# Kernel tuning notes

Measured on AMD Instinct MI355X. Metric: run time of the kernel, lower is better.

## Reference

```python
import jax, jax.numpy as jnp
import numpy as np

B, T = 16384, 64
VOCAB, D, HD, FF = 10, 3, 4, 2
EPS = 1e-6


def _rms(x, w):
    return x * jax.lax.rsqrt(jnp.mean(x * x, axis=-1, keepdims=True) + EPS) * w


def _rope(x, theta=3.0):
    # x: [..., T, HD]; interleaved rotary, matching the torch RotaryEmbedding
    t = jnp.arange(x.shape[-2], dtype=x.dtype)
    inv_freq = 1.0 / theta ** (jnp.arange(0, HD, 2, dtype=x.dtype) / HD)  # [HD/2]
    freqs = jnp.outer(t, inv_freq)                                        # [T, HD/2]
    cos_f, sin_f = jnp.cos(freqs), jnp.sin(freqs)
    x1, x2 = x[..., ::2], x[..., 1::2]
    rot = jnp.stack([x1 * cos_f - x2 * sin_f, x1 * sin_f + x2 * cos_f], axis=-1)
    return rot.reshape(x.shape)


def setup_inputs() -> dict:
    key = jax.random.key(0)
    ks = jax.random.split(key, 12)
    f32 = jnp.float32
    return {
        "idx": jax.random.randint(ks[0], (B, T), 0, VOCAB, dtype=jnp.int32),
        "arc_A": jnp.asarray(2.5, f32),
        "arc_start": jnp.asarray(-1.2, f32),
        "arc_stride": jnp.asarray(0.29, f32),
        "w_ln1": jnp.ones((D,), f32) + 0.1 * jax.random.normal(ks[1], (D,), f32),
        "w_ln2": jnp.ones((D,), f32) + 0.1 * jax.random.normal(ks[2], (D,), f32),
        "w_lnf": jnp.ones((D,), f32) + 0.1 * jax.random.normal(ks[3], (D,), f32),
        "w_qn": jnp.ones((HD,), f32) + 0.1 * jax.random.normal(ks[4], (HD,), f32),
        "Wq": jax.random.normal(ks[5], (HD, D), f32) * 0.5,
        "Wk": jax.random.normal(ks[6], (HD, D), f32) * 0.5,
        "Wg": jax.random.normal(ks[7], (FF, D), f32) * 0.5,
        "Wu": jax.random.normal(ks[8], (FF, D), f32) * 0.5,
        "Wd": jax.random.normal(ks[9], (D, FF), f32) * 0.5,
    }


def reference(idx, arc_A, arc_start, arc_stride, w_ln1, w_ln2, w_lnf, w_qn,
              Wq, Wk, Wg, Wu, Wd):
    dt = arc_A.dtype
    # circular-arc token embedding table [VOCAB, 2]
    digits = jnp.arange(VOCAB, dtype=dt)
    angles = arc_start + digits * arc_stride
    table = jnp.stack([arc_A * jnp.cos(angles), arc_A * jnp.sin(angles)], axis=1)

    tok = table[idx]                                              # [B,T,2]
    pe = jnp.sin(jnp.arange(T, dtype=dt) * jnp.exp(jnp.asarray(-np.log(10000.0), dt)))
    pos = jnp.broadcast_to(pe[None, :, None], (idx.shape[0], T, 1))
    x = jnp.concatenate([tok, pos], axis=-1)                      # [B,T,3]

    h = _rms(x, w_ln1)
    q = _rms(h @ Wq.T, w_qn)                                      # [B,T,HD]
    k = _rms(h @ Wk.T, w_qn)
    v = h @ Wk.T                                                  # v = k pre-norm? no: v = k.clone() BEFORE q_norm
    q = _rope(q)
    k = _rope(k)

    scale = HD ** (-0.5)
    scores = jnp.einsum("btd,bsd->bts", q, k) * scale             # [B,T,T]
    causal = jnp.triu(jnp.ones((T, T), dtype=bool), k=1)
    scores = jnp.where(causal, -jnp.inf, scores)
    attn = jax.nn.softmax(scores, axis=-1)
    out = jnp.einsum("bts,bsd->btd", attn, v)                     # [B,T,HD]

    x = x + out @ Wq                                              # F.linear(out, Wq.T) == out @ Wq
    h = _rms(x, w_ln2)
    x = x + (jax.nn.silu(h @ Wg.T) * (h @ Wu.T)) @ Wd.T
    x = _rms(x, w_lnf)
    return x[..., :2] @ table.T                                   # [B,T,VOCAB]
```

## Files before the change

kernel.cpp:

```cpp
#include <hip/hip_runtime.h>
#include <math.h>


namespace {
constexpr int kVocab = 10;
constexpr float kEps = 1e-6f;
constexpr int kWaves = 4;

typedef __attribute__((ext_vector_type(8)))  short short8;
typedef __attribute__((ext_vector_type(16))) float float16;

constexpr int kOffQh  = 0;
constexpr int kOffQl  = 512;
constexpr int kOffKh  = 1024;
constexpr int kOffKl  = 1536;
constexpr int kOffVt  = 2048;
constexpr int kOffO   = 3200;
constexpr int kWaveLds = 4736;
constexpr int kVtP = 72;
constexpr int kOP  = 76;

__device__ __forceinline__ unsigned bf16_1(float a) {
    return (__float_as_uint(a) + 0x8000u) >> 16;
}
__device__ __forceinline__ unsigned pk_bf16(float a, float b) {
    const unsigned au = __float_as_uint(a) + 0x8000u;
    const unsigned bu = __float_as_uint(b) + 0x8000u;
    return (au >> 16) | (bu & 0xffff0000u);
}
__device__ __forceinline__ float bf_lo(unsigned u) { return __uint_as_float(u << 16); }
__device__ __forceinline__ float bf_hi(unsigned u) { return __uint_as_float(u & 0xffff0000u); }

__device__ __forceinline__ float16 mfma(short8 a, short8 b, float16 c) {
    return __builtin_amdgcn_mfma_f32_32x32x16_bf16(a, b, c, 0, 0, 0);
}

__device__ __forceinline__ short8 tok_frag(const char* wbase, int off, int tok, bool lo_half) {
    uint2 r = *(const uint2*)(wbase + off + tok * 8);
    uint4 t;
    t.x = lo_half ? r.x : 0u;
    t.y = lo_half ? r.y : 0u;
    t.z = 0u; t.w = 0u;
    return __builtin_bit_cast(short8, t);
}

template<bool MASKED>
__device__ __forceinline__ void exp_pack(const float16& S, unsigned* out, int m) {
#pragma unroll
    for (int i = 0; i < 8; ++i) {
        const int r0 = 2 * i, r1 = 2 * i + 1;
        float sa = S[r0], sb = S[r1];
        if (MASKED) {
            sa = (((r0 & 3) + 8 * (r0 >> 2)) <= m) ? sa : -INFINITY;
            sb = (((r1 & 3) + 8 * (r1 >> 2)) <= m) ? sb : -INFINITY;
        }
        out[i] = pk_bf16(__builtin_amdgcn_exp2f(sa), __builtin_amdgcn_exp2f(sb));
    }
}

__device__ __forceinline__ short8 af(const unsigned* p) {
    uint4 t;
    t.x = p[0]; t.y = p[1]; t.z = p[2]; t.w = p[3];
    return __builtin_bit_cast(short8, t);
}
__device__ __forceinline__ short8 ld8(const void* p) {
    return __builtin_bit_cast(short8, *(const uint4*)p);
}

__global__ __launch_bounds__(256, 4) void adder_model_kernel(
    const int* __restrict__ idx,
    const float* __restrict__ p_arcA,
    const float* __restrict__ p_arcStart,
    const float* __restrict__ p_arcStride,
    const float* __restrict__ w_ln1,
    const float* __restrict__ w_ln2,
    const float* __restrict__ w_lnf,
    const float* __restrict__ w_qn,
    const float* __restrict__ Wq,
    const float* __restrict__ Wk,
    const float* __restrict__ Wg,
    const float* __restrict__ Wu,
    const float* __restrict__ Wd,
    float* __restrict__ out)
{
    __shared__ __align__(16) char smem[kWaves][kWaveLds];
    __shared__ __align__(16) float table_s[kVocab * 2];

    const int lane = threadIdx.x & 63;
    const int wid  = threadIdx.x >> 6;
    char* wbase = &smem[wid][0];

    if (threadIdx.x < kVocab) {
        const float ang = p_arcStart[0] + (float)threadIdx.x * p_arcStride[0];
        const float A = p_arcA[0];
        table_s[2 * threadIdx.x]     = A * __cosf(ang);
        table_s[2 * threadIdx.x + 1] = A * __sinf(ang);
    }
    __syncthreads();

    const float t_f = (float)lane;
    const float pe  = __sinf(t_f * 1e-4f);
    const float c0  = __cosf(t_f);
    const float s0  = __sinf(t_f);
    const float ang1 = t_f * 0.57735026918962576f;
    const float c1  = __cosf(ang1);
    const float s1  = __sinf(ang1);

    const float wl1_0 = w_ln1[0], wl1_1 = w_ln1[1], wl1_2 = w_ln1[2];
    const float wl2_0 = w_ln2[0], wl2_1 = w_ln2[1], wl2_2 = w_ln2[2];
    const float wlf0 = w_lnf[0], wlf1 = w_lnf[1];
    const float wqn0 = w_qn[0], wqn1 = w_qn[1], wqn2 = w_qn[2], wqn3 = w_qn[3];
    const float Wq00 = Wq[0],  Wq01 = Wq[1],  Wq02 = Wq[2];
    const float Wq10 = Wq[3],  Wq11 = Wq[4],  Wq12 = Wq[5];
    const float Wq20 = Wq[6],  Wq21 = Wq[7],  Wq22 = Wq[8];
    const float Wq30 = Wq[9],  Wq31 = Wq[10], Wq32 = Wq[11];
    const float Wk00 = Wk[0],  Wk01 = Wk[1],  Wk02 = Wk[2];
    const float Wk10 = Wk[3],  Wk11 = Wk[4],  Wk12 = Wk[5];
    const float Wk20 = Wk[6],  Wk21 = Wk[7],  Wk22 = Wk[8];
    const float Wk30 = Wk[9],  Wk31 = Wk[10], Wk32 = Wk[11];
    const float Wg00 = Wg[0],  Wg01 = Wg[1],  Wg02 = Wg[2];
    const float Wg10 = Wg[3],  Wg11 = Wg[4],  Wg12 = Wg[5];
    const float Wu00 = Wu[0],  Wu01 = Wu[1],  Wu02 = Wu[2];
    const float Wu10 = Wu[3],  Wu11 = Wu[4],  Wu12 = Wu[5];
    const float Wd00 = Wd[0],  Wd01 = Wd[1];
    const float Wd10 = Wd[2],  Wd11 = Wd[3];
    const float Wd20 = Wd[4],  Wd21 = Wd[5];

    const int row = (int)blockIdx.x * kWaves + wid;

    const int tix = idx[(size_t)row * 64 + lane];
    const float2 emb = *(const float2*)(table_s + 2 * tix);
    const float x0i = emb.x, x1i = emb.y, x2i = pe;

    const float r1 = __builtin_amdgcn_rsqf((x0i*x0i + x1i*x1i + x2i*x2i) * (1.0f/3.0f) + kEps);
    const float h0 = x0i * r1 * wl1_0;
    const float h1 = x1i * r1 * wl1_1;
    const float h2 = x2i * r1 * wl1_2;

    const float qp0 = h0*Wq00 + h1*Wq01 + h2*Wq02;
    const float qp1 = h0*Wq10 + h1*Wq11 + h2*Wq12;
    const float qp2 = h0*Wq20 + h1*Wq21 + h2*Wq22;
    const float qp3 = h0*Wq30 + h1*Wq31 + h2*Wq32;
    const float v0 = h0*Wk00 + h1*Wk01 + h2*Wk02;
    const float v1 = h0*Wk10 + h1*Wk11 + h2*Wk12;
    const float v2 = h0*Wk20 + h1*Wk21 + h2*Wk22;
    const float v3 = h0*Wk30 + h1*Wk31 + h2*Wk32;

    const float rq = __builtin_amdgcn_rsqf((qp0*qp0 + qp1*qp1 + qp2*qp2 + qp3*qp3) * 0.25f + kEps);
    const float rk = __builtin_amdgcn_rsqf((v0*v0 + v1*v1 + v2*v2 + v3*v3) * 0.25f + kEps);
    const float qn0 = qp0*rq*wqn0, qn1 = qp1*rq*wqn1, qn2 = qp2*rq*wqn2, qn3 = qp3*rq*wqn3;
    const float kn0 = v0*rk*wqn0,  kn1 = v1*rk*wqn1,  kn2 = v2*rk*wqn2,  kn3 = v3*rk*wqn3;

    constexpr float kQS = 0.72134752044448170f;
    const float q0 = (qn0*c0 - qn1*s0) * kQS;
    const float q1 = (qn0*s0 + qn1*c0) * kQS;
    const float q2 = (qn2*c1 - qn3*s1) * kQS;
    const float q3 = (qn2*s1 + qn3*c1) * kQS;
    const float k0 = kn0*c0 - kn1*s0;
    const float k1 = kn0*s0 + kn1*c0;
    const float k2 = kn2*c1 - kn3*s1;
    const float k3 = kn2*s1 + kn3*c1;

    uint2 qh, ql, kh, kl;
    qh.x = pk_bf16(q0, q1); qh.y = pk_bf16(q2, q3);
    ql.x = pk_bf16(q0 - bf_lo(qh.x), q1 - bf_hi(qh.x));
    ql.y = pk_bf16(q2 - bf_lo(qh.y), q3 - bf_hi(qh.y));
    kh.x = pk_bf16(k0, k1); kh.y = pk_bf16(k2, k3);
    kl.x = pk_bf16(k0 - bf_lo(kh.x), k1 - bf_hi(kh.x));
    kl.y = pk_bf16(k2 - bf_lo(kh.y), k3 - bf_hi(kh.y));
    *(uint2*)(wbase + kOffQh + lane * 8) = qh;
    *(uint2*)(wbase + kOffQl + lane * 8) = ql;
    *(uint2*)(wbase + kOffKh + lane * 8) = kh;
    *(uint2*)(wbase + kOffKl + lane * 8) = kl;

    ushort* Vt = (ushort*)(wbase + kOffVt);
    const int vcol = (lane & ~12) | ((lane & 4) << 1) | ((lane & 8) >> 1);
    Vt[0 * kVtP + vcol] = (ushort)bf16_1(v0);
    Vt[1 * kVtP + vcol] = (ushort)bf16_1(v1);
    Vt[2 * kVtP + vcol] = (ushort)bf16_1(v2);
    Vt[3 * kVtP + vcol] = (ushort)bf16_1(v3);
    Vt[4 * kVtP + vcol] = (ushort)0x3F80;
    __threadfence_block();

    const int  tloc = lane & 31;
    const bool loh  = lane < 32;
    const int  h    = lane >> 5;
    const int  m    = tloc - 4 * h;

    const short8 aKh0 = tok_frag(wbase, kOffKh, tloc,      loh);
    const short8 aKl0 = tok_frag(wbase, kOffKl, tloc,      loh);
    const short8 aKh1 = tok_frag(wbase, kOffKh, tloc + 32, loh);
    const short8 aKl1 = tok_frag(wbase, kOffKl, tloc + 32, loh);
    const short8 bQh0 = tok_frag(wbase, kOffQh, tloc,      loh);
    const short8 bQl0 = tok_frag(wbase, kOffQl, tloc,      loh);
    const short8 bQh1 = tok_frag(wbase, kOffQh, tloc + 32, loh);
    const short8 bQl1 = tok_frag(wbase, kOffQl, tloc + 32, loh);

    short8 vb[4];
#pragma unroll
    for (int kc = 0; kc < 4; ++kc)
        vb[kc] = ld8(Vt + (tloc & 7) * kVtP + 16 * kc + 8 * h);

    float16 Z = {0,0,0,0,0,0,0,0,0,0,0,0,0,0,0,0};
    float16 S00 = mfma(aKl0, bQh0, mfma(aKh0, bQl0, mfma(aKh0, bQh0, Z)));
    float16 S01 = mfma(aKl0, bQh1, mfma(aKh0, bQl1, mfma(aKh0, bQh1, Z)));
    float16 S11 = mfma(aKl1, bQh1, mfma(aKh1, bQl1, mfma(aKh1, bQh1, Z)));

    unsigned p00[8], p01[8], p11[8];
    exp_pack<true >(S00, p00, m);
    exp_pack<false>(S01, p01, m);
    exp_pack<true >(S11, p11, m);

    float16 acc0 = mfma(af(p00 + 4), vb[1], mfma(af(p00), vb[0], Z));
    float16 acc1 = mfma(af(p11 + 4), vb[3],
                   mfma(af(p11),     vb[2],
                   mfma(af(p01 + 4), vb[1],
                   mfma(af(p01),     vb[0], Z))));

    float* Ol = (float*)(wbase + kOffO);
    if (tloc < 5) {
#pragma unroll
        for (int c = 0; c < 4; ++c) {
            float4 w0 = make_float4(acc0[4*c], acc0[4*c+1], acc0[4*c+2], acc0[4*c+3]);
            *(float4*)(Ol + tloc * kOP +      8 * c + 4 * h) = w0;
            float4 w1 = make_float4(acc1[4*c], acc1[4*c+1], acc1[4*c+2], acc1[4*c+3]);
            *(float4*)(Ol + tloc * kOP + 32 + 8 * c + 4 * h) = w1;
        }
    }
    __threadfence_block();

    const float o0r = Ol[0 * kOP + lane];
    const float o1r = Ol[1 * kOP + lane];
    const float o2r = Ol[2 * kOP + lane];
    const float o3r = Ol[3 * kOP + lane];
    const float lr  = Ol[4 * kOP + lane];

    const float invl = __builtin_amdgcn_rcpf(lr);
    const float o0 = o0r * invl, o1 = o1r * invl, o2 = o2r * invl, o3 = o3r * invl;

    const float xa0 = x0i + o0*Wq00 + o1*Wq10 + o2*Wq20 + o3*Wq30;
    const float xa1 = x1i + o0*Wq01 + o1*Wq11 + o2*Wq21 + o3*Wq31;
    const float xa2 = x2i + o0*Wq02 + o1*Wq12 + o2*Wq22 + o3*Wq32;

    const float r2 = __builtin_amdgcn_rsqf((xa0*xa0 + xa1*xa1 + xa2*xa2) * (1.0f/3.0f) + kEps);
    const float hh0 = xa0*r2*wl2_0, hh1 = xa1*r2*wl2_1, hh2 = xa2*r2*wl2_2;
    const float g0 = hh0*Wg00 + hh1*Wg01 + hh2*Wg02;
    const float g1 = hh0*Wg10 + hh1*Wg11 + hh2*Wg12;
    const float u0 = hh0*Wu00 + hh1*Wu01 + hh2*Wu02;
    const float u1 = hh0*Wu10 + hh1*Wu11 + hh2*Wu12;
    constexpr float kL2E = 1.4426950408889634f;
    const float f0 = g0 * __builtin_amdgcn_rcpf(1.0f + __builtin_amdgcn_exp2f(-g0 * kL2E)) * u0;
    const float f1 = g1 * __builtin_amdgcn_rcpf(1.0f + __builtin_amdgcn_exp2f(-g1 * kL2E)) * u1;
    const float xf0 = xa0 + f0*Wd00 + f1*Wd01;
    const float xf1 = xa1 + f0*Wd10 + f1*Wd11;
    const float xf2 = xa2 + f0*Wd20 + f1*Wd21;

    const float rf = __builtin_amdgcn_rsqf((xf0*xf0 + xf1*xf1 + xf2*xf2) * (1.0f/3.0f) + kEps);
    const float y0 = xf0 * rf * wlf0;
    const float y1 = xf1 * rf * wlf1;

    const float4* tb4 = (const float4*)table_s;
    const float4 T0 = tb4[0], T1 = tb4[1], T2 = tb4[2], T3 = tb4[3], T4 = tb4[4];

    float2* op = (float2*)(out + (size_t)(row * 64 + lane) * kVocab);
    op[0] = float2{y0*T0.x + y1*T0.y, y0*T0.z + y1*T0.w};
    op[1] = float2{y0*T1.x + y1*T1.y, y0*T1.z + y1*T1.w};
    op[2] = float2{y0*T2.x + y1*T2.y, y0*T2.z + y1*T2.w};
    op[3] = float2{y0*T3.x + y1*T3.y, y0*T3.z + y1*T3.w};
    op[4] = float2{y0*T4.x + y1*T4.y, y0*T4.z + y1*T4.w};
}
}

extern "C" void kernel_launch(void* const* d_in, const int* in_sizes, int n_in,
                              void* d_out, int out_size, void* d_ws, size_t ws_size,
                              hipStream_t stream) {
    (void)in_sizes; (void)n_in; (void)d_ws; (void)ws_size; (void)out_size;
    const int*   idx       = (const int*)  d_in[0];
    const float* arcA      = (const float*)d_in[1];
    const float* arcStart  = (const float*)d_in[2];
    const float* arcStride = (const float*)d_in[3];
    const float* w_ln1     = (const float*)d_in[4];
    const float* w_ln2     = (const float*)d_in[5];
    const float* w_lnf     = (const float*)d_in[6];
    const float* w_qn      = (const float*)d_in[7];
    const float* Wq        = (const float*)d_in[8];
    const float* Wk        = (const float*)d_in[9];
    const float* Wg        = (const float*)d_in[10];
    const float* Wu        = (const float*)d_in[11];
    const float* Wd        = (const float*)d_in[12];
    float* out = (float*)d_out;

    dim3 grid(4096), block(256);
    hipLaunchKernelGGL(adder_model_kernel, grid, block, 0, stream,
                       idx, arcA, arcStart, arcStride,
                       w_ln1, w_ln2, w_lnf, w_qn, Wq, Wk, Wg, Wu, Wd, out);
}
```

Baseline: 106.3 us.

## Replace LDS staging of Q/K fragments and attention output with cross-lane shuffles

Q/K hi/lo fragments are no longer written to and read back from LDS. They are built from registers, with a 32-lane xor shuffle supplying the second token half. The PV MFMA operands are swapped so the output lands transposed, and a few shuffles pull the per-token output and normaliser straight from the accumulators, dropping the O scratch buffer and one LDS round trip. Per-wave LDS shrinks to just the V^T tile, which is padded with zero rows. This can improve occupancy, but the correctness of the new lane mapping is subtle.

```diff
diff --git a/kernel.cpp b/kernel.cpp
--- a/kernel.cpp
+++ b/kernel.cpp
@@ -10,15 +10,8 @@
 typedef __attribute__((ext_vector_type(8)))  short short8;
 typedef __attribute__((ext_vector_type(16))) float float16;
 
-constexpr int kOffQh  = 0;
-constexpr int kOffQl  = 512;
-constexpr int kOffKh  = 1024;
-constexpr int kOffKl  = 1536;
-constexpr int kOffVt  = 2048;
-constexpr int kOffO   = 3200;
-constexpr int kWaveLds = 4736;
 constexpr int kVtP = 72;
-constexpr int kOP  = 76;
+constexpr int kWaveLds = 1152;
 
 __device__ __forceinline__ unsigned bf16_1(float a) {
     return (__float_as_uint(a) + 0x8000u) >> 16;
@@ -34,14 +27,19 @@
 __device__ __forceinline__ float16 mfma(short8 a, short8 b, float16 c) {
     return __builtin_amdgcn_mfma_f32_32x32x16_bf16(a, b, c, 0, 0, 0);
 }
-
-__device__ __forceinline__ short8 tok_frag(const char* wbase, int off, int tok, bool lo_half) {
-    uint2 r = *(const uint2*)(wbase + off + tok * 8);
+__device__ __forceinline__ unsigned shflx32(unsigned x) {
+    return (unsigned)__shfl_xor((int)x, 32, 64);
+}
+
+__device__ __forceinline__ short8 mk_frag(uint2 v, bool lo) {
     uint4 t;
-    t.x = lo_half ? r.x : 0u;
-    t.y = lo_half ? r.y : 0u;
+    t.x = lo ? v.x : 0u;
+    t.y = lo ? v.y : 0u;
     t.z = 0u; t.w = 0u;
     return __builtin_bit_cast(short8, t);
+}
+__device__ __forceinline__ short8 ld8(const void* p) {
+    return __builtin_bit_cast(short8, *(const uint4*)p);
 }
 
 template<bool MASKED>
@@ -62,9 +60,6 @@
     uint4 t;
     t.x = p[0]; t.y = p[1]; t.z = p[2]; t.w = p[3];
     return __builtin_bit_cast(short8, t);
-}
-__device__ __forceinline__ short8 ld8(const void* p) {
-    return __builtin_bit_cast(short8, *(const uint4*)p);
 }
 
 __global__ __launch_bounds__(256, 4) void adder_model_kernel(
@@ -88,7 +83,7 @@
 
     const int lane = threadIdx.x & 63;
     const int wid  = threadIdx.x >> 6;
-    char* wbase = &smem[wid][0];
+    ushort* Vt = (ushort*)&smem[wid][0];
 
     if (threadIdx.x < kVocab) {
         const float ang = p_arcStart[0] + (float)threadIdx.x * p_arcStride[0];
@@ -168,33 +163,38 @@
     kh.x = pk_bf16(k0, k1); kh.y = pk_bf16(k2, k3);
     kl.x = pk_bf16(k0 - bf_lo(kh.x), k1 - bf_hi(kh.x));
     kl.y = pk_bf16(k2 - bf_lo(kh.y), k3 - bf_hi(kh.y));
-    *(uint2*)(wbase + kOffQh + lane * 8) = qh;
-    *(uint2*)(wbase + kOffQl + lane * 8) = ql;
-    *(uint2*)(wbase + kOffKh + lane * 8) = kh;
-    *(uint2*)(wbase + kOffKl + lane * 8) = kl;
-
-    ushort* Vt = (ushort*)(wbase + kOffVt);
+
     const int vcol = (lane & ~12) | ((lane & 4) << 1) | ((lane & 8) >> 1);
     Vt[0 * kVtP + vcol] = (ushort)bf16_1(v0);
     Vt[1 * kVtP + vcol] = (ushort)bf16_1(v1);
     Vt[2 * kVtP + vcol] = (ushort)bf16_1(v2);
     Vt[3 * kVtP + vcol] = (ushort)bf16_1(v3);
     Vt[4 * kVtP + vcol] = (ushort)0x3F80;
-    __threadfence_block();
+    Vt[5 * kVtP + vcol] = 0;
+    Vt[6 * kVtP + vcol] = 0;
+    Vt[7 * kVtP + vcol] = 0;
+
+    uint2 qh1, ql1, kh1, kl1;
+    qh1.x = shflx32(qh.x); qh1.y = shflx32(qh.y);
+    ql1.x = shflx32(ql.x); ql1.y = shflx32(ql.y);
+    kh1.x = shflx32(kh.x); kh1.y = shflx32(kh.y);
+    kl1.x = shflx32(kl.x); kl1.y = shflx32(kl.y);
 
     const int  tloc = lane & 31;
     const bool loh  = lane < 32;
     const int  h    = lane >> 5;
     const int  m    = tloc - 4 * h;
 
-    const short8 aKh0 = tok_frag(wbase, kOffKh, tloc,      loh);
-    const short8 aKl0 = tok_frag(wbase, kOffKl, tloc,      loh);
-    const short8 aKh1 = tok_frag(wbase, kOffKh, tloc + 32, loh);
-    const short8 aKl1 = tok_frag(wbase, kOffKl, tloc + 32, loh);
-    const short8 bQh0 = tok_frag(wbase, kOffQh, tloc,      loh);
-    const short8 bQl0 = tok_frag(wbase, kOffQl, tloc,      loh);
-    const short8 bQh1 = tok_frag(wbase, kOffQh, tloc + 32, loh);
-    const short8 bQl1 = tok_frag(wbase, kOffQl, tloc + 32, loh);
+    const short8 aKh0 = mk_frag(kh,  loh);
+    const short8 aKl0 = mk_frag(kl,  loh);
+    const short8 aKh1 = mk_frag(kh1, loh);
+    const short8 aKl1 = mk_frag(kl1, loh);
+    const short8 bQh0 = mk_frag(qh,  loh);
+    const short8 bQl0 = mk_frag(ql,  loh);
+    const short8 bQh1 = mk_frag(qh1, loh);
+    const short8 bQl1 = mk_frag(ql1, loh);
+
+    __threadfence_block();
 
     short8 vb[4];
 #pragma unroll
@@ -211,29 +211,21 @@
     exp_pack<false>(S01, p01, m);
     exp_pack<true >(S11, p11, m);
 
-    float16 acc0 = mfma(af(p00 + 4), vb[1], mfma(af(p00), vb[0], Z));
-    float16 acc1 = mfma(af(p11 + 4), vb[3],
-                   mfma(af(p11),     vb[2],
-                   mfma(af(p01 + 4), vb[1],
-                   mfma(af(p01),     vb[0], Z))));
-
-    float* Ol = (float*)(wbase + kOffO);
-    if (tloc < 5) {
-#pragma unroll
-        for (int c = 0; c < 4; ++c) {
-            float4 w0 = make_float4(acc0[4*c], acc0[4*c+1], acc0[4*c+2], acc0[4*c+3]);
-            *(float4*)(Ol + tloc * kOP +      8 * c + 4 * h) = w0;
-            float4 w1 = make_float4(acc1[4*c], acc1[4*c+1], acc1[4*c+2], acc1[4*c+3]);
-            *(float4*)(Ol + tloc * kOP + 32 + 8 * c + 4 * h) = w1;
-        }
-    }
-    __threadfence_block();
-
-    const float o0r = Ol[0 * kOP + lane];
-    const float o1r = Ol[1 * kOP + lane];
-    const float o2r = Ol[2 * kOP + lane];
-    const float o3r = Ol[3 * kOP + lane];
-    const float lr  = Ol[4 * kOP + lane];
+    float16 acc0 = mfma(vb[1], af(p00 + 4), mfma(vb[0], af(p00), Z));
+    float16 acc1 = mfma(vb[3], af(p11 + 4),
+                   mfma(vb[2], af(p11),
+                   mfma(vb[1], af(p01 + 4),
+                   mfma(vb[0], af(p01), Z))));
+
+    const float e0 = __shfl_xor(loh ? acc1[0] : acc0[0], 32, 64);
+    const float e1 = __shfl_xor(loh ? acc1[1] : acc0[1], 32, 64);
+    const float e2 = __shfl_xor(loh ? acc1[2] : acc0[2], 32, 64);
+    const float e3 = __shfl_xor(loh ? acc1[3] : acc0[3], 32, 64);
+    const float o0r = loh ? acc0[0] : e0;
+    const float o1r = loh ? acc0[1] : e1;
+    const float o2r = loh ? acc0[2] : e2;
+    const float o3r = loh ? acc0[3] : e3;
+    const float lr  = loh ? e0 : acc1[0];
 
     const float invl = __builtin_amdgcn_rcpf(lr);
     const float o0 = o0r * invl, o1 = o1r * invl, o2 = o2r * invl, o3 = o3r * invl;
```

New measurement: 106.2 us. No clear change (-0.2%).
